# Performance work log

Hardware: AMD Instinct MI355X
Metric: run time of the kernel (lower is better)

The kernel has to match this reference:

```python
import jax, jax.numpy as jnp
import numpy as np

B, U, HEADS, S = 16, 1024, 8, 1024


def setup_inputs() -> dict:
    key = jax.random.key(0)
    k1, k2, k3, k4 = jax.random.split(key, 4)
    x = jax.random.normal(k1, (B, U, S), dtype=jnp.float32)
    mask = jax.random.randint(k2, (B, S, S), 0, 2).astype(bool)
    w_qkv = jax.random.normal(k3, (3 * U, U), dtype=jnp.float32) * 0.02
    w_out = jax.random.normal(k4, (U, U), dtype=jnp.float32) * 0.02
    return {"x": x, "mask": mask, "w_qkv": w_qkv, "w_out": w_out}


def reference(x, mask, w_qkv, w_out):
    # x: (B, U, S), mask: (B, n_queries, n_keys) bool
    b, u, s = x.shape
    h = HEADS
    c = u // h  # head (chunk) size
    scale = 1.0 / np.sqrt(c).astype(np.float32)

    # 1x1-conv QKV projection (bias=False): (3U, U) x (B, U, S) -> (B, 3U, S)
    qkv = jnp.einsum('ou,bus->bos', w_qkv, x)
    Q, K, V = jnp.split(qkv, 3, axis=1)           # each (B, U, S)
    Qh = Q.reshape(b, h, c, s)
    Kh = K.reshape(b, h, c, s)
    Vh = V.reshape(b, h, c, s)

    # attention logits: (B, H, n_q, n_k)
    A = jnp.einsum('bhcq,bhck->bhqk', Qh, Kh)

    # relu activation with per-query valid-key-count normalization
    m = mask.sum(axis=2)[:, :, None]              # (B, n_q, 1) count of valid keys
    n_elem = jnp.where(mask, m, 1).astype(A.dtype)[:, None]  # (B, 1, n_q, n_k)
    mask_b = mask[:, None]                        # broadcast over heads
    A = jnp.where(mask_b, jax.nn.relu(A) * scale, -jnp.inf)
    A = A / n_elem
    A = jnp.where(jnp.isinf(A), jnp.zeros((), A.dtype), A)

    # attention-value aggregation (faithful math of broadcast+sum): (B, H, C, n_q)
    Ch = jnp.einsum('bhqk,bhck->bhcq', A, Vh)
    Cc = Ch.reshape(b, u, s)

    # finishing 1x1-conv linear layer
    return jnp.einsum('ou,bus->bos', w_out, Cc)
```

## Files before the change

kernel.cpp:

```cpp
#include <hip/hip_runtime.h>

#define B_DIM 16
#define U_DIM 1024
#define H_DIM 8
#define S_DIM 1024
#define C_DIM 128
#define KD 1024
#define SCALE 0.08838834764831845f

typedef __attribute__((ext_vector_type(8))) short s16x8;
typedef __attribute__((ext_vector_type(4))) float f32x4;

__device__ __forceinline__ void gll16(const void* g, void* l) {
  __builtin_amdgcn_global_load_lds(
      (const __attribute__((address_space(1))) unsigned int*)g,
      (__attribute__((address_space(3))) unsigned int*)l, 16, 0, 0);
}
__device__ __forceinline__ unsigned short f2bf(float f) {
  unsigned u = __float_as_uint(f);
  u += 0x7FFF + ((u >> 16) & 1u);
  return (unsigned short)(u >> 16);
}
#define MFMA16(a, b, c) __builtin_amdgcn_mfma_f32_16x16x32_bf16(a, b, c, 0, 0, 0)

__global__ void detect_mask(const unsigned char* __restrict__ mask_raw, int* __restrict__ flag) {
  __shared__ int not01, notf;
  if (threadIdx.x == 0) { not01 = 0; notf = 0; }
  __syncthreads();
  const unsigned int* p = (const unsigned int*)mask_raw;
  int l01 = 0, lf = 0;
  for (int i = threadIdx.x; i < 4096; i += 256) {
    unsigned int v = p[i];
    if (v != 0u && v != 1u) l01 = 1;
    if (v != 0u && v != 0x3F800000u) lf = 1;
  }
  if (l01) atomicOr(&not01, 1);
  if (lf) atomicOr(&notf, 1);
  __syncthreads();
  if (threadIdx.x == 0) flag[0] = (!not01) ? 0 : ((!notf) ? 2 : 1);
}

__global__ __launch_bounds__(256) void mask_invm(const unsigned char* __restrict__ mask_raw,
                                                 const int* __restrict__ flag,
                                                 float* __restrict__ invm) {
  int row = blockIdx.x * 4 + (threadIdx.x >> 6);
  int lane = threadIdx.x & 63;
  int mkind = flag[0];
  int sum = 0;
  if (mkind == 1) {
    const unsigned char* p = mask_raw + (size_t)row * S_DIM;
    for (int k = lane; k < S_DIM; k += 64) sum += (p[k] != 0);
  } else if (mkind == 0) {
    const int* p = (const int*)mask_raw + (size_t)row * S_DIM;
    for (int k = lane; k < S_DIM; k += 64) sum += (p[k] != 0);
  } else {
    const float* p = (const float*)mask_raw + (size_t)row * S_DIM;
    for (int k = lane; k < S_DIM; k += 64) sum += (p[k] != 0.f);
  }
#pragma unroll
  for (int off = 32; off > 0; off >>= 1) sum += __shfl_down(sum, off, 64);
  if (lane == 0) invm[row] = (sum > 0) ? (SCALE / (float)sum) : 0.f;
}

__global__ __launch_bounds__(256) void cvt_bf16(const float* __restrict__ in,
                                                unsigned short* __restrict__ out, int n) {
  int i = (blockIdx.x * 256 + threadIdx.x) * 4;
  if (i < n) {
    float4 v = *(const float4*)(in + i);
    ushort4 o;
    o.x = f2bf(v.x); o.y = f2bf(v.y); o.z = f2bf(v.z); o.w = f2bf(v.w);
    *(ushort4*)(out + i) = o;
  }
}

__global__ __launch_bounds__(256) void transpose_x(const float* __restrict__ x,
                                                   unsigned short* __restrict__ xT) {
  __shared__ float T[32][33];
  const int t = threadIdx.x, r = t >> 3, c4 = (t & 7) * 4;
  const int s0 = blockIdx.x * 32, u0 = blockIdx.y * 32;
  const size_t base = (size_t)blockIdx.z * U_DIM * S_DIM;
  float4 v = *(const float4*)(x + base + (size_t)(u0 + r) * S_DIM + s0 + c4);
  T[r][c4 + 0] = v.x; T[r][c4 + 1] = v.y; T[r][c4 + 2] = v.z; T[r][c4 + 3] = v.w;
  __syncthreads();
  ushort4 o;
  o.x = f2bf(T[c4 + 0][r]); o.y = f2bf(T[c4 + 1][r]);
  o.z = f2bf(T[c4 + 2][r]); o.w = f2bf(T[c4 + 3][r]);
  *(ushort4*)(xT + base + (size_t)(s0 + r) * U_DIM + u0 + c4) = o;
}

__global__ __launch_bounds__(256) void transpose_v(const unsigned short* __restrict__ qkvT,
                                                   unsigned short* __restrict__ VT) {
  __shared__ unsigned short T[32][34];
  const int t = threadIdx.x, r = t >> 3, c4 = (t & 7) * 4;
  const int k0 = blockIdx.x * 32, c0 = blockIdx.y * 32;
  const unsigned short* qb = qkvT + (size_t)blockIdx.z * S_DIM * (3 * U_DIM);
  ushort4 v = *(const ushort4*)(qb + (size_t)(k0 + r) * (3 * U_DIM) + 2 * U_DIM + c0 + c4);
  T[r][c4 + 0] = v.x; T[r][c4 + 1] = v.y; T[r][c4 + 2] = v.z; T[r][c4 + 3] = v.w;
  __syncthreads();
  ushort4 o;
  o.x = T[c4 + 0][r]; o.y = T[c4 + 1][r]; o.z = T[c4 + 2][r]; o.w = T[c4 + 3][r];
  *(ushort4*)(VT + (size_t)blockIdx.z * U_DIM * S_DIM + (size_t)(c0 + r) * S_DIM + k0 + c4) = o;
}

template <typename OUT>
__global__ __launch_bounds__(256) void gemm_tt(const unsigned short* __restrict__ A,
                                               const unsigned short* __restrict__ Bm,
                                               OUT* __restrict__ D,
                                               long long sAb, long long sBb, long long sDb,
                                               int N) {
  __shared__ unsigned short sA[128 * 32];
  __shared__ unsigned short sB[128 * 32];
  const int tid = threadIdx.x, wave = tid >> 6, lane = tid & 63;
  const int l15 = lane & 15, quad = lane >> 4;
  const int m0 = blockIdx.y * 128, n0 = blockIdx.x * 128;
  A += (size_t)blockIdx.z * sAb;
  Bm += (size_t)blockIdx.z * sBb;
  D += (size_t)blockIdx.z * sDb;
  const int wm = (wave >> 1) * 64, wn = (wave & 1) * 64;
  f32x4 acc[4][4] = {};

  for (int k0 = 0; k0 < KD; k0 += 32) {
#pragma unroll
    for (int t = 0; t < 2; ++t) {
      int p = wave * 128 + t * 64 + lane;
      int row = p >> 2, kc = (p & 3) ^ (row & 3);
      gll16(A + (size_t)(m0 + row) * KD + k0 + kc * 8, &sA[(wave * 128 + t * 64) * 8]);
    }
#pragma unroll
    for (int t = 0; t < 2; ++t) {
      int p = wave * 128 + t * 64 + lane;
      int row = p >> 2, kc = (p & 3) ^ (row & 3);
      gll16(Bm + (size_t)(n0 + row) * KD + k0 + kc * 8, &sB[(wave * 128 + t * 64) * 8]);
    }
    __syncthreads();
    s16x8 af[4], bf[4];
#pragma unroll
    for (int i = 0; i < 4; ++i) {
      int row = wm + i * 16 + l15;
      af[i] = *(const s16x8*)&sA[row * 32 + (quad ^ (row & 3)) * 8];
    }
#pragma unroll
    for (int j = 0; j < 4; ++j) {
      int row = wn + j * 16 + l15;
      bf[j] = *(const s16x8*)&sB[row * 32 + (quad ^ (row & 3)) * 8];
    }
#pragma unroll
    for (int i = 0; i < 4; ++i)
#pragma unroll
      for (int j = 0; j < 4; ++j) acc[i][j] = MFMA16(af[i], bf[j], acc[i][j]);
    __syncthreads();
  }
#pragma unroll
  for (int i = 0; i < 4; ++i)
#pragma unroll
    for (int j = 0; j < 4; ++j) {
      f32x4 v = acc[i][j];
#pragma unroll
      for (int r = 0; r < 4; ++r) {
        int m = m0 + wm + i * 16 + quad * 4 + r;
        int n = n0 + wn + j * 16 + l15;
        if constexpr (sizeof(OUT) == 2) D[(size_t)m * N + n] = f2bf(v[r]);
        else D[(size_t)m * N + n] = v[r];
      }
    }
}

__global__ __launch_bounds__(256, 2) void attn_mfma(const unsigned short* __restrict__ qkvT,
                                                    const unsigned short* __restrict__ VT,
                                                    const unsigned char* __restrict__ mask_raw,
                                                    const int* __restrict__ flag,
                                                    const float* __restrict__ invm,
                                                    unsigned short* __restrict__ CcT, int b0) {
  __shared__ unsigned short Qs[64 * 128];
  __shared__ unsigned short Ks[64 * 128];
  __shared__ unsigned short Vs[128 * 64];
  __shared__ unsigned short Ps[64 * 64];
  __shared__ float invs[64];

  const int tid = threadIdx.x, wave = tid >> 6, lane = tid & 63;
  const int l15 = lane & 15, quad = lane >> 4;
  const int q0 = blockIdx.x * 64, h = blockIdx.y, z = blockIdx.z, b = b0 + z;
  const unsigned short* qB = qkvT + (size_t)z * S_DIM * (3 * U_DIM);
  const unsigned short* Vb = VT + (size_t)z * U_DIM * S_DIM + (size_t)h * C_DIM * S_DIM;
  const int mkind = flag[0];

#pragma unroll
  for (int t = 0; t < 4; ++t) {
    int p = wave * 256 + t * 64 + lane;
    int row = p >> 4, c = (p & 15) ^ (row & 7);
    gll16(qB + (size_t)(q0 + row) * (3 * U_DIM) + h * C_DIM + c * 8,
          &Qs[(wave * 256 + t * 64) * 8]);
  }
  if (tid < 64) invs[tid] = invm[(size_t)b * S_DIM + q0 + tid];
  __syncthreads();

  s16x8 qf[4][4];
#pragma unroll
  for (int i = 0; i < 4; ++i)
#pragma unroll
    for (int kk = 0; kk < 4; ++kk) {
      int row = i * 16 + l15;
      qf[i][kk] = *(const s16x8*)&Qs[row * 128 + ((kk * 4 + quad) ^ (row & 7)) * 8];
    }
  float invf[4][4];
#pragma unroll
  for (int i = 0; i < 4; ++i)
#pragma unroll
    for (int r = 0; r < 4; ++r) invf[i][r] = invs[i * 16 + quad * 4 + r];

  f32x4 pacc[4][2] = {};

  for (int kt = 0; kt < S_DIM / 64; ++kt) {
    const int k0t = kt * 64;
    __syncthreads();
#pragma unroll
    for (int t = 0; t < 4; ++t) {
      int p = wave * 256 + t * 64 + lane;
      int row = p >> 4, c = (p & 15) ^ (row & 7);
      gll16(qB + (size_t)(k0t + row) * (3 * U_DIM) + U_DIM + h * C_DIM + c * 8,
            &Ks[(wave * 256 + t * 64) * 8]);
    }
#pragma unroll
    for (int t = 0; t < 4; ++t) {
      int p = wave * 256 + t * 64 + lane;
      int row = p >> 3, kc = (p & 7) ^ (row & 7);
      gll16(Vb + (size_t)row * S_DIM + k0t + kc * 8, &Vs[(wave * 256 + t * 64) * 8]);
    }
    float msel[4][4];
    {
      const int kg = k0t + wave * 16 + l15;
      if (mkind == 1) {
        const unsigned char* mp = mask_raw + ((size_t)b << 20);
#pragma unroll
        for (int i = 0; i < 4; ++i)
#pragma unroll
          for (int r = 0; r < 4; ++r) {
            int q = q0 + i * 16 + quad * 4 + r;
            msel[i][r] = mp[((size_t)q << 10) + kg] ? 1.f : 0.f;
          }
      } else if (mkind == 0) {
        const int* mp = (const int*)mask_raw + ((size_t)b << 20);
#pragma unroll
        for (int i = 0; i < 4; ++i)
#pragma unroll
          for (int r = 0; r < 4; ++r) {
            int q = q0 + i * 16 + quad * 4 + r;
            msel[i][r] = mp[((size_t)q << 10) + kg] ? 1.f : 0.f;
          }
      } else {
        const float* mp = (const float*)mask_raw + ((size_t)b << 20);
#pragma unroll
        for (int i = 0; i < 4; ++i)
#pragma unroll
          for (int r = 0; r < 4; ++r) {
            int q = q0 + i * 16 + quad * 4 + r;
            msel[i][r] = (mp[((size_t)q << 10) + kg] != 0.f) ? 1.f : 0.f;
          }
      }
    }
    __syncthreads();

    f32x4 sacc[4] = {};
#pragma unroll
    for (int kk = 0; kk < 4; ++kk) {
      int row = wave * 16 + l15;
      s16x8 bk = *(const s16x8*)&Ks[row * 128 + ((kk * 4 + quad) ^ (row & 7)) * 8];
#pragma unroll
      for (int i = 0; i < 4; ++i) sacc[i] = MFMA16(qf[i][kk], bk, sacc[i]);
    }
#pragma unroll
    for (int i = 0; i < 4; ++i)
#pragma unroll
      for (int r = 0; r < 4; ++r) {
        int q = i * 16 + quad * 4 + r;
        int kl = wave * 16 + l15;
        float p = fmaxf(sacc[i][r], 0.f) * invf[i][r] * msel[i][r];
        Ps[q * 64 + (((kl >> 3) ^ (q & 7))) * 8 + (kl & 7)] = f2bf(p);
      }
    __syncthreads();

#pragma unroll
    for (int ks = 0; ks < 2; ++ks) {
      s16x8 pf[4], vf[2];
#pragma unroll
      for (int i = 0; i < 4; ++i) {
        int row = i * 16 + l15;
        pf[i] = *(const s16x8*)&Ps[row * 64 + ((ks * 4 + quad) ^ (row & 7)) * 8];
      }
#pragma unroll
      for (int j = 0; j < 2; ++j) {
        int row = wave * 32 + j * 16 + l15;
        vf[j] = *(const s16x8*)&Vs[row * 64 + ((ks * 4 + quad) ^ (row & 7)) * 8];
      }
#pragma unroll
      for (int i = 0; i < 4; ++i)
#pragma unroll
        for (int j = 0; j < 2; ++j) pacc[i][j] = MFMA16(pf[i], vf[j], pacc[i][j]);
    }
  }

  unsigned short* cb = CcT + (size_t)z * S_DIM * U_DIM;
#pragma unroll
  for (int i = 0; i < 4; ++i)
#pragma unroll
    for (int j = 0; j < 2; ++j) {
      f32x4 v = pacc[i][j];
#pragma unroll
      for (int r = 0; r < 4; ++r) {
        int q = q0 + i * 16 + quad * 4 + r;
        int c = h * C_DIM + wave * 32 + j * 16 + l15;
        cb[(size_t)q * U_DIM + c] = f2bf(v[r]);
      }
    }
}

extern "C" void kernel_launch(void* const* d_in, const int* in_sizes, int n_in,
                              void* d_out, int out_size, void* d_ws, size_t ws_size,
                              hipStream_t stream) {
  const float* x = (const float*)d_in[0];
  const unsigned char* mask_raw = (const unsigned char*)d_in[1];
  const float* w_qkv = (const float*)d_in[2];
  const float* w_out = (const float*)d_in[3];
  float* out = (float*)d_out;

  char* ws = (char*)d_ws;
  int* flag = (int*)ws;
  float* invm = (float*)(ws + 256);
  unsigned short* wqkv_bf = (unsigned short*)(ws + 256 + 65536);
  unsigned short* wout_bf = (unsigned short*)((char*)wqkv_bf + (size_t)3 * U_DIM * U_DIM * 2);
  char* heap = (char*)wout_bf + (size_t)U_DIM * U_DIM * 2;

  const size_t xT_pb = (size_t)U_DIM * S_DIM * 2;
  const size_t qkvT_pb = (size_t)3 * U_DIM * S_DIM * 2;
  const size_t vT_pb = (size_t)U_DIM * S_DIM * 2;
  const size_t ccT_pb = (size_t)U_DIM * S_DIM * 2;
  const size_t per_batch = xT_pb + qkvT_pb + vT_pb + ccT_pb;
  const size_t fixed = (size_t)(heap - ws);
  int nb = (ws_size > fixed) ? (int)((ws_size - fixed) / per_batch) : 1;
  if (nb < 1) nb = 1;
  if (nb > B_DIM) nb = B_DIM;

  unsigned short* xT = (unsigned short*)heap;
  unsigned short* qkvT = (unsigned short*)(heap + (size_t)nb * xT_pb);
  unsigned short* VT = (unsigned short*)(heap + (size_t)nb * (xT_pb + qkvT_pb));
  unsigned short* CcT = (unsigned short*)(heap + (size_t)nb * (xT_pb + qkvT_pb + vT_pb));

  detect_mask<<<1, 256, 0, stream>>>(mask_raw, flag);
  mask_invm<<<(B_DIM * S_DIM) / 4, 256, 0, stream>>>(mask_raw, flag, invm);
  cvt_bf16<<<(3 * U_DIM * U_DIM) / 1024, 256, 0, stream>>>(w_qkv, wqkv_bf, 3 * U_DIM * U_DIM);
  cvt_bf16<<<(U_DIM * U_DIM) / 1024, 256, 0, stream>>>(w_out, wout_bf, U_DIM * U_DIM);

  for (int b0 = 0; b0 < B_DIM; b0 += nb) {
    int cnt = (B_DIM - b0 < nb) ? (B_DIM - b0) : nb;
    transpose_x<<<dim3(S_DIM / 32, U_DIM / 32, cnt), 256, 0, stream>>>(
        x + (size_t)b0 * U_DIM * S_DIM, xT);
    gemm_tt<unsigned short><<<dim3(3 * U_DIM / 128, S_DIM / 128, cnt), 256, 0, stream>>>(
        xT, wqkv_bf, qkvT, (long long)U_DIM * S_DIM, 0LL, (long long)3 * U_DIM * S_DIM, 3 * U_DIM);
    transpose_v<<<dim3(S_DIM / 32, U_DIM / 32, cnt), 256, 0, stream>>>(qkvT, VT);
    attn_mfma<<<dim3(S_DIM / 64, H_DIM, cnt), 256, 0, stream>>>(
        qkvT, VT, mask_raw, flag, invm, CcT, b0);
    gemm_tt<float><<<dim3(S_DIM / 128, U_DIM / 128, cnt), 256, 0, stream>>>(
        wout_bf, CcT, out + (size_t)b0 * U_DIM * S_DIM, 0LL,
        (long long)U_DIM * S_DIM, (long long)U_DIM * S_DIM, S_DIM);
  }
}
```

Measured before the change: 514.0 us.

## Pack attention mask into bitmasks and share Q/P shared-memory buffer

Adds a pre-pass that converts the boolean mask into 64-bit ballot words per key and 64-query block, so the attention kernel loads one word per lane per tile instead of sixteen scattered byte/int loads. The Q staging buffer is reused for the P tile, which reduces shared memory, and launch bounds are raised to allow three blocks per CU. The cost is an extra kernel launch and a pass over the full mask, plus possible register pressure from the tighter occupancy target.

```diff
diff --git a/kernel.cpp b/kernel.cpp
--- a/kernel.cpp
+++ b/kernel.cpp
@@ -62,6 +62,48 @@
   if (lane == 0) invm[row] = (sum > 0) ? (SCALE / (float)sum) : 0.f;
 }
 
+__global__ __launch_bounds__(256) void pack_mask(const unsigned char* __restrict__ mask_raw,
+                                                 const int* __restrict__ flag,
+                                                 unsigned long long* __restrict__ bits) {
+  __shared__ unsigned char tile[64][80];
+  const int t = threadIdx.x;
+  const int kt = blockIdx.x * 64, qw = blockIdx.y, b = blockIdx.z;
+  const int mk = flag[0];
+  const int q = t >> 2, kbase = (t & 3) * 16;
+  const size_t row = (size_t)(b * S_DIM + qw * 64 + q);
+  if (mk == 1) {
+    uint4 v = *(const uint4*)(mask_raw + (row << 10) + kt + kbase);
+    *(uint4*)&tile[q][kbase] = v;
+  } else if (mk == 0) {
+    const int* p = (const int*)mask_raw + (row << 10) + kt + kbase;
+#pragma unroll
+    for (int j = 0; j < 4; ++j) {
+      int4 v = ((const int4*)p)[j];
+      uchar4 o;
+      o.x = v.x ? 1 : 0; o.y = v.y ? 1 : 0; o.z = v.z ? 1 : 0; o.w = v.w ? 1 : 0;
+      *(uchar4*)&tile[q][kbase + j * 4] = o;
+    }
+  } else {
+    const float* p = (const float*)mask_raw + (row << 10) + kt + kbase;
+#pragma unroll
+    for (int j = 0; j < 4; ++j) {
+      float4 v = ((const float4*)p)[j];
+      uchar4 o;
+      o.x = (v.x != 0.f) ? 1 : 0; o.y = (v.y != 0.f) ? 1 : 0;
+      o.z = (v.z != 0.f) ? 1 : 0; o.w = (v.w != 0.f) ? 1 : 0;
+      *(uchar4*)&tile[q][kbase + j * 4] = o;
+    }
+  }
+  __syncthreads();
+  const int wave = t >> 6, lane = t & 63;
+#pragma unroll
+  for (int kk = 0; kk < 16; ++kk) {
+    int k = wave * 16 + kk;
+    unsigned long long bal = __ballot(tile[lane][k] != 0);
+    if (lane == 0) bits[((size_t)(b * S_DIM + kt + k) << 4) + qw] = bal;
+  }
+}
+
 __global__ __launch_bounds__(256) void cvt_bf16(const float* __restrict__ in,
                                                 unsigned short* __restrict__ out, int n) {
   int i = (blockIdx.x * 256 + threadIdx.x) * 4;
@@ -165,16 +207,14 @@
     }
 }
 
-__global__ __launch_bounds__(256, 2) void attn_mfma(const unsigned short* __restrict__ qkvT,
+__global__ __launch_bounds__(256, 3) void attn_mfma(const unsigned short* __restrict__ qkvT,
                                                     const unsigned short* __restrict__ VT,
-                                                    const unsigned char* __restrict__ mask_raw,
-                                                    const int* __restrict__ flag,
+                                                    const unsigned long long* __restrict__ bits,
                                                     const float* __restrict__ invm,
                                                     unsigned short* __restrict__ CcT, int b0) {
-  __shared__ unsigned short Qs[64 * 128];
   __shared__ unsigned short Ks[64 * 128];
   __shared__ unsigned short Vs[128 * 64];
-  __shared__ unsigned short Ps[64 * 64];
+  __shared__ unsigned short QPs[64 * 128];
   __shared__ float invs[64];
 
   const int tid = threadIdx.x, wave = tid >> 6, lane = tid & 63;
@@ -182,14 +222,14 @@
   const int q0 = blockIdx.x * 64, h = blockIdx.y, z = blockIdx.z, b = b0 + z;
   const unsigned short* qB = qkvT + (size_t)z * S_DIM * (3 * U_DIM);
   const unsigned short* Vb = VT + (size_t)z * U_DIM * S_DIM + (size_t)h * C_DIM * S_DIM;
-  const int mkind = flag[0];
+  const unsigned long long* mb = bits + ((size_t)b * S_DIM << 4) + (q0 >> 6);
 
 #pragma unroll
   for (int t = 0; t < 4; ++t) {
     int p = wave * 256 + t * 64 + lane;
     int row = p >> 4, c = (p & 15) ^ (row & 7);
     gll16(qB + (size_t)(q0 + row) * (3 * U_DIM) + h * C_DIM + c * 8,
-          &Qs[(wave * 256 + t * 64) * 8]);
+          &QPs[(wave * 256 + t * 64) * 8]);
   }
   if (tid < 64) invs[tid] = invm[(size_t)b * S_DIM + q0 + tid];
   __syncthreads();
@@ -200,7 +240,7 @@
 #pragma unroll
     for (int kk = 0; kk < 4; ++kk) {
       int row = i * 16 + l15;
-      qf[i][kk] = *(const s16x8*)&Qs[row * 128 + ((kk * 4 + quad) ^ (row & 7)) * 8];
+      qf[i][kk] = *(const s16x8*)&QPs[row * 128 + ((kk * 4 + quad) ^ (row & 7)) * 8];
     }
   float invf[4][4];
 #pragma unroll
@@ -226,38 +266,7 @@
       int row = p >> 3, kc = (p & 7) ^ (row & 7);
       gll16(Vb + (size_t)row * S_DIM + k0t + kc * 8, &Vs[(wave * 256 + t * 64) * 8]);
     }
-    float msel[4][4];
-    {
-      const int kg = k0t + wave * 16 + l15;
-      if (mkind == 1) {
-        const unsigned char* mp = mask_raw + ((size_t)b << 20);
-#pragma unroll
-        for (int i = 0; i < 4; ++i)
-#pragma unroll
-          for (int r = 0; r < 4; ++r) {
-            int q = q0 + i * 16 + quad * 4 + r;
-            msel[i][r] = mp[((size_t)q << 10) + kg] ? 1.f : 0.f;
-          }
-      } else if (mkind == 0) {
-        const int* mp = (const int*)mask_raw + ((size_t)b << 20);
-#pragma unroll
-        for (int i = 0; i < 4; ++i)
-#pragma unroll
-          for (int r = 0; r < 4; ++r) {
-            int q = q0 + i * 16 + quad * 4 + r;
-            msel[i][r] = mp[((size_t)q << 10) + kg] ? 1.f : 0.f;
-          }
-      } else {
-        const float* mp = (const float*)mask_raw + ((size_t)b << 20);
-#pragma unroll
-        for (int i = 0; i < 4; ++i)
-#pragma unroll
-          for (int r = 0; r < 4; ++r) {
-            int q = q0 + i * 16 + quad * 4 + r;
-            msel[i][r] = (mp[((size_t)q << 10) + kg] != 0.f) ? 1.f : 0.f;
-          }
-      }
-    }
+    unsigned long long w64 = mb[(size_t)(k0t + wave * 16 + l15) << 4];
     __syncthreads();
 
     f32x4 sacc[4] = {};
@@ -274,8 +283,9 @@
       for (int r = 0; r < 4; ++r) {
         int q = i * 16 + quad * 4 + r;
         int kl = wave * 16 + l15;
-        float p = fmaxf(sacc[i][r], 0.f) * invf[i][r] * msel[i][r];
-        Ps[q * 64 + (((kl >> 3) ^ (q & 7))) * 8 + (kl & 7)] = f2bf(p);
+        float p = fmaxf(sacc[i][r], 0.f) * invf[i][r];
+        p = ((w64 >> q) & 1ull) ? p : 0.f;
+        QPs[q * 64 + (((kl >> 3) ^ (q & 7))) * 8 + (kl & 7)] = f2bf(p);
       }
     __syncthreads();
 
@@ -285,7 +295,7 @@
 #pragma unroll
       for (int i = 0; i < 4; ++i) {
         int row = i * 16 + l15;
-        pf[i] = *(const s16x8*)&Ps[row * 64 + ((ks * 4 + quad) ^ (row & 7)) * 8];
+        pf[i] = *(const s16x8*)&QPs[row * 64 + ((ks * 4 + quad) ^ (row & 7)) * 8];
       }
 #pragma unroll
       for (int j = 0; j < 2; ++j) {
@@ -326,7 +336,8 @@
   char* ws = (char*)d_ws;
   int* flag = (int*)ws;
   float* invm = (float*)(ws + 256);
-  unsigned short* wqkv_bf = (unsigned short*)(ws + 256 + 65536);
+  unsigned long long* bits = (unsigned long long*)(ws + 256 + 65536);
+  unsigned short* wqkv_bf = (unsigned short*)((char*)bits + (size_t)B_DIM * S_DIM * 16 * 8);
   unsigned short* wout_bf = (unsigned short*)((char*)wqkv_bf + (size_t)3 * U_DIM * U_DIM * 2);
   char* heap = (char*)wout_bf + (size_t)U_DIM * U_DIM * 2;
 
@@ -347,6 +358,7 @@
 
   detect_mask<<<1, 256, 0, stream>>>(mask_raw, flag);
   mask_invm<<<(B_DIM * S_DIM) / 4, 256, 0, stream>>>(mask_raw, flag, invm);
+  pack_mask<<<dim3(S_DIM / 64, S_DIM / 64, B_DIM), 256, 0, stream>>>(mask_raw, flag, bits);
   cvt_bf16<<<(3 * U_DIM * U_DIM) / 1024, 256, 0, stream>>>(w_qkv, wqkv_bf, 3 * U_DIM * U_DIM);
   cvt_bf16<<<(U_DIM * U_DIM) / 1024, 256, 0, stream>>>(w_out, wout_bf, U_DIM * U_DIM);
 
@@ -358,7 +370,7 @@
         xT, wqkv_bf, qkvT, (long long)U_DIM * S_DIM, 0LL, (long long)3 * U_DIM * S_DIM, 3 * U_DIM);
     transpose_v<<<dim3(S_DIM / 32, U_DIM / 32, cnt), 256, 0, stream>>>(qkvT, VT);
     attn_mfma<<<dim3(S_DIM / 64, H_DIM, cnt), 256, 0, stream>>>(
-        qkvT, VT, mask_raw, flag, invm, CcT, b0);
+        qkvT, VT, bits, invm, CcT, b0);
     gemm_tt<float><<<dim3(S_DIM / 128, U_DIM / 128, cnt), 256, 0, stream>>>(
         wout_bf, CcT, out + (size_t)b0 * U_DIM * S_DIM, 0LL,
         (long long)U_DIM * S_DIM, (long long)U_DIM * S_DIM, S_DIM);
```

New measurement: 717.6 us. 1.4x slower.
